# Optimization experiments

Hardware: AMD Instinct MI355X
Metric: run time of the kernel (lower is better)

Reference implementation:

```python
import jax, jax.numpy as jnp
import numpy as np

DIM = 256; QK = 256; HEADS = 8; TOPK = 2; WV = 2; WH = 2
SCALE = QK ** -0.5


def setup_inputs() -> dict:
    key = jax.random.key(0)
    ks = jax.random.split(key, 6)
    x = jax.random.normal(ks[0], (4, DIM, 64, 64), jnp.float32)
    Wqkv = jax.random.normal(ks[1], (DIM, 2 * QK + DIM), jnp.float32) * 0.02
    bqkv = jnp.zeros((2 * QK + DIM,), jnp.float32)
    Wo = jax.random.normal(ks[2], (DIM, DIM), jnp.float32) * 0.02
    bo = jnp.zeros((DIM,), jnp.float32)
    lepe_w = jax.random.normal(ks[3], (3, 3, 1, DIM), jnp.float32) * 0.1  # HWIO depthwise
    lepe_b = jnp.zeros((DIM,), jnp.float32)
    return {"x": x, "Wqkv": Wqkv, "bqkv": bqkv, "Wo": Wo, "bo": bo,
            "lepe_w": lepe_w, "lepe_b": lepe_b}


def _dwconv(x, w, b):
    # depthwise 3x3 conv, NHWC
    y = jax.lax.conv_general_dilated(x, w, (1, 1), 'SAME',
                                     dimension_numbers=('NHWC', 'HWIO', 'NHWC'),
                                     feature_group_count=x.shape[-1])
    return y + b


def _branch(win, Wqkv, bqkv, lepe_w, lepe_b, to_image):
    n, p2, h, w, _ = win.shape
    w2 = h * w
    qkv = win @ Wqkv + bqkv
    q = qkv[..., :QK]
    kv = qkv[..., QK:]                                  # [n,p2,h,w,QK+DIM]
    q_pix = q.reshape(n, p2, w2, QK)
    kv_pix = kv.reshape(n, p2, w2, QK + DIM)            # identity kv_down
    # region routing (detached in original)
    q_win = jax.lax.stop_gradient(q).mean((2, 3))       # [n,p2,QK]
    k_win = jax.lax.stop_gradient(kv[..., :QK]).mean((2, 3))
    logit = jnp.einsum('npc,nqc->npq', q_win * SCALE, k_win)
    _, r_idx = jax.lax.top_k(logit, TOPK)               # [n,p2,TOPK]
    # gather selected KV windows (mul_weight='none')
    kv_sel = jax.vmap(lambda kvb, idxb: kvb[idxb])(kv_pix, r_idx)  # [n,p2,k,w2,ckv]
    k_sel = kv_sel[..., :QK].reshape(n, p2, TOPK * w2, HEADS, QK // HEADS)
    v_sel = kv_sel[..., QK:].reshape(n, p2, TOPK * w2, HEADS, DIM // HEADS)
    qh = q_pix.reshape(n, p2, w2, HEADS, QK // HEADS)
    attn = jax.nn.softmax(jnp.einsum('npqhd,npkhd->nphqk', qh * SCALE, k_sel), axis=-1)
    out = jnp.einsum('nphqk,npkhd->npqhd', attn, v_sel).reshape(n, p2, h, w, DIM)
    lepe = _dwconv(to_image(kv[..., QK:]), lepe_w, lepe_b)
    return to_image(out) + lepe


def reference(x, Wqkv, bqkv, Wo, bo, lepe_w, lepe_b):
    xh = x.transpose(0, 2, 3, 1)                        # NHWC
    N, H, W, C = xh.shape
    v_win, h_win = H // WV, W // WH
    # vertical branch: horizontal strips of height WV, full width
    vm = xh.reshape(N, v_win, WV, W, C)
    # horizontal branch: vertical strips of width WH, full height
    hm = xh.reshape(N, H, h_win, WH, C).transpose(0, 2, 1, 3, 4)
    img_v = lambda a: a.reshape(N, H, W, a.shape[-1])
    img_h = lambda a: a.transpose(0, 2, 1, 3, 4).reshape(N, H, W, a.shape[-1])
    o1 = _branch(vm, Wqkv, bqkv, lepe_w, lepe_b, img_v)
    o2 = _branch(hm, Wqkv, bqkv, lepe_w, lepe_b, img_h)
    out = (o1 @ Wo + bo) + (o2 @ Wo + bo)
    return out.transpose(0, 3, 1, 2)                    # back to NCHW
```

## Files before the change

### kernel.cpp

```cpp
#include <hip/hip_runtime.h>
#include <hip/hip_bf16.h>
#include <math.h>

#define NBATCH 4
#define HW     4096
#define NPIX   16384
#define SCALE  0.0625f
#define QLOG2E (0.0625f * 1.44269504088896340736f)

typedef __attribute__((ext_vector_type(8))) short bf16x8;
typedef __attribute__((ext_vector_type(4))) float f32x4;

__device__ __forceinline__ int pixmap(int b, int n, int p, int pos){
  return (b == 0) ? (n*HW + p*128 + pos)
                  : (n*HW + (pos >> 1)*64 + (p << 1) + (pos & 1));
}

__device__ __forceinline__ ushort f2b(float x){
  __hip_bfloat16 h = __float2bfloat16(x);
  return *reinterpret_cast<ushort*>(&h);
}
__device__ __forceinline__ float b2f(ushort u){
  __hip_bfloat16 h = *reinterpret_cast<__hip_bfloat16*>(&u);
  return __bfloat162float(h);
}
__device__ __forceinline__ uint pk2(float a, float b){
  return (uint)f2b(a) | ((uint)f2b(b) << 16);
}

__global__ __launch_bounds__(256) void k_xt(
    const float* __restrict__ x, ushort* __restrict__ Xb)
{
  __shared__ float T[32][257];
  const int n = blockIdx.y, hw0 = blockIdx.x * 32;
  const int tid = threadIdx.x;
  const int hl = tid & 31, cg = tid >> 5;
  #pragma unroll 8
  for(int i = 0; i < 32; i++){
    const int c = i*8 + cg;
    T[hl][c] = x[((size_t)(n*256 + c))*4096 + hw0 + hl];
  }
  __syncthreads();
  const int c0 = (tid & 31)*8, pb = tid >> 5;
  #pragma unroll
  for(int i = 0; i < 4; i++){
    const int p = pb + 8*i;
    union { bf16x8 v; ushort u[8]; } U;
    #pragma unroll
    for(int j = 0; j < 8; j++) U.u[j] = f2b(T[p][c0 + j]);
    *(bf16x8*)(Xb + ((size_t)(n*HW + hw0 + p))*256 + c0) = U.v;
  }
}

__global__ __launch_bounds__(256) void k_wt(
    const float* __restrict__ Wqkv, ushort* __restrict__ Wt)
{
  const int o = blockIdx.x, t = threadIdx.x;
  Wt[(size_t)o*256 + t] = f2b(Wqkv[(size_t)t*768 + o]);
}

__global__ __launch_bounds__(256) void k_wto(
    const float* __restrict__ Wo, ushort* __restrict__ WoT)
{
  const int o = blockIdx.x, t = threadIdx.x;
  WoT[(size_t)o*256 + t] = f2b(Wo[(size_t)t*256 + o]);
}

__global__ __launch_bounds__(256) void k_qkv_mfma(
    const ushort* __restrict__ Xb, const ushort* __restrict__ Wt,
    const float* __restrict__ bqkv, ushort* __restrict__ QKVb)
{
  const int tid = threadIdx.x;
  const int l = tid & 63, w = tid >> 6;
  const int wr = w >> 1, wc = w & 1;
  const int q16 = l & 15, g = l >> 4;
  const int row0 = blockIdx.x*128 + wr*64;
  const int col0 = blockIdx.y*128 + wc*64;

  f32x4 acc[4][4];
  #pragma unroll
  for(int i = 0; i < 4; i++)
    #pragma unroll
    for(int j = 0; j < 4; j++) acc[i][j] = (f32x4){0,0,0,0};

  const ushort* Ab = Xb + (size_t)(row0 + q16)*256 + 8*g;
  const ushort* Bb = Wt + (size_t)(col0 + q16)*256 + 8*g;

  #pragma unroll
  for(int ks = 0; ks < 8; ks++){
    const int k0 = ks*32;
    bf16x8 a[4], b[4];
    #pragma unroll
    for(int i = 0; i < 4; i++) a[i] = *(const bf16x8*)(Ab + (size_t)(16*i)*256 + k0);
    #pragma unroll
    for(int j = 0; j < 4; j++) b[j] = *(const bf16x8*)(Bb + (size_t)(16*j)*256 + k0);
    #pragma unroll
    for(int i = 0; i < 4; i++)
      #pragma unroll
      for(int j = 0; j < 4; j++)
        acc[i][j] = __builtin_amdgcn_mfma_f32_16x16x32_bf16(a[i], b[j], acc[i][j], 0, 0, 0);
  }

  #pragma unroll
  for(int j = 0; j < 4; j++){
    const int col = col0 + 16*j + q16;
    const float bias = bqkv[col];
    const float sc = (col < 256) ? QLOG2E : 1.f;
    #pragma unroll
    for(int i = 0; i < 4; i++){
      #pragma unroll
      for(int r = 0; r < 4; r++){
        const int row = row0 + 16*i + 4*g + r;
        QKVb[(size_t)row*768 + col] = f2b((acc[i][j][r] + bias) * sc);
      }
    }
  }
}

__global__ __launch_bounds__(256) void k_vt(
    const ushort* __restrict__ QKVb, ushort* __restrict__ Vt)
{
  __shared__ ushort T[32][258];
  const int tile = blockIdx.x;
  const int n = tile >> 7;
  const int hw0 = (tile & 127) * 32;
  const int tid = threadIdx.x;
  #pragma unroll 4
  for(int i = 0; i < 32; i++)
    T[i][tid] = QKVb[(size_t)(n*HW + hw0 + i)*768 + 512 + tid];
  __syncthreads();
  const int px = tid & 31, wv = tid >> 5;
  #pragma unroll 4
  for(int ccb = 0; ccb < 32; ccb++){
    const int c = ccb*8 + wv;
    Vt[((size_t)(n*256 + c))*4096 + hw0 + px] = T[px][c];
  }
}

__global__ __launch_bounds__(256) void k_xmean(
    const float* __restrict__ x, float* __restrict__ xwin)
{
  const int n = blockIdx.y;
  const int c = blockIdx.x*4 + (threadIdx.x >> 6);
  const int l = threadIdx.x & 63;
  const float* xc = x + ((size_t)(n*256 + c))*4096;

  float csum = 0.f;
  for(int h = 0; h < 64; h++) csum += xc[h*64 + l];
  float rsum = 0.f;
  const float4* xr = (const float4*)(xc + l*64);
  #pragma unroll 4
  for(int i = 0; i < 16; i++){ const float4 v = xr[i]; rsum += (v.x+v.y)+(v.z+v.w); }

  const int p = l & 31;
  const float rp = __shfl(rsum, 2*p) + __shfl(rsum, 2*p + 1);
  const float cp = __shfl(csum, 2*p) + __shfl(csum, 2*p + 1);
  if(l < 32){
    xwin[((size_t)((0*NBATCH + n)*32 + p))*256 + c] = rp * (1.f/128.f);
    xwin[((size_t)((1*NBATCH + n)*32 + p))*256 + c] = cp * (1.f/128.f);
  }
}

__global__ __launch_bounds__(256) void k_win_gemm(
    const float* __restrict__ xwin, const float* __restrict__ Wqkv,
    const float* __restrict__ bqkv, float* __restrict__ qwin, float* __restrict__ kwin)
{
  __shared__ float xs[256];
  const int row = blockIdx.x;
  const int tid = threadIdx.x;
  xs[tid] = xwin[(size_t)row*256 + tid];
  __syncthreads();
  #pragma unroll
  for(int half = 0; half < 2; half++){
    const int col = half*256 + tid;
    float s = 0.f;
    for(int k = 0; k < 256; k++) s += xs[k] * Wqkv[(size_t)k*768 + col];
    s += bqkv[col];
    if(half == 0) qwin[(size_t)row*256 + tid] = s;
    else          kwin[(size_t)row*256 + tid] = s;
  }
}

__global__ __launch_bounds__(256) void k_logits_top2(
    const float* __restrict__ qwin, const float* __restrict__ kwin, int* __restrict__ ridx)
{
  const int n = blockIdx.x, b = blockIdx.y;
  __shared__ float lg[32][32];
  const int base = ((b*NBATCH + n)*32)*256;
  for(int t = threadIdx.x; t < 1024; t += 256){
    const int p = t >> 5, q = t & 31;
    const float* qp = qwin + base + p*256;
    const float* kq = kwin + base + q*256;
    float s = 0.f;
    for(int c = 0; c < 256; c++) s += qp[c]*kq[c];
    lg[p][q] = s * SCALE;
  }
  __syncthreads();
  if(threadIdx.x < 32){
    const int p = threadIdx.x;
    float m0 = -INFINITY; int i0 = 0;
    for(int q = 0; q < 32; q++){ const float v = lg[p][q]; if(v > m0){ m0 = v; i0 = q; } }
    float m1 = -INFINITY; int i1 = 0;
    for(int q = 0; q < 32; q++){ if(q == i0) continue; const float v = lg[p][q]; if(v > m1){ m1 = v; i1 = q; } }
    const int o = ((b*NBATCH + n)*32 + p)*2;
    ridx[o] = i0; ridx[o+1] = i1;
  }
}

__global__ __launch_bounds__(64) void k_attn_mfma(
    const ushort* __restrict__ QKVb, const ushort* __restrict__ Vt,
    const int* __restrict__ ridx, ushort* __restrict__ Ob)
{
  int id = blockIdx.x;
  const int hd = id & 7;  id >>= 3;
  const int p  = id & 31; id >>= 5;
  const int n  = id & 3;  id >>= 2;
  const int b  = id;
  const int l = threadIdx.x;
  const int q16 = l & 15, g = l >> 4;

  const int ro = ((b*NBATCH + n)*32 + p)*2;
  const int r0 = ridx[ro], r1 = ridx[ro+1];

  int qpix[8];
  bf16x8 qf[8];
  #pragma unroll
  for(int m = 0; m < 8; m++){
    qpix[m] = pixmap(b, n, p, m*16 + q16);
    qf[m] = *(const bf16x8*)(QKVb + (size_t)qpix[m]*768 + hd*32 + 8*g);
  }

  f32x4 acc0[8], acc1[8];
  float rs[8];
  #pragma unroll
  for(int m = 0; m < 8; m++){
    acc0[m] = (f32x4){0,0,0,0}; acc1[m] = (f32x4){0,0,0,0}; rs[m] = 0.f;
  }

  const int e = g & 1, t = g >> 1;
  const int a0 = (q16 + 32*e) << 2;
  const int a1 = (q16 + 32*e + 16) << 2;

  for(int c = 0; c < 8; c++){
    const int wsel = (c < 4) ? r0 : r1;
    const int posb = (32*c) & 127;

    bf16x8 kf0, kf1;
    {
      const int kp0 = pixmap(b, n, wsel, posb + q16);
      kf0 = *(const bf16x8*)(QKVb + (size_t)kp0*768 + 256 + hd*32 + 8*g);
      const int kp1 = pixmap(b, n, wsel, posb + 16 + q16);
      kf1 = *(const bf16x8*)(QKVb + (size_t)kp1*768 + 256 + hd*32 + 8*g);
    }
    bf16x8 vf0, vf1;
    if(b == 0){
      const ushort* base = Vt + ((size_t)(n*256 + hd*32 + q16))*4096 + wsel*128 + posb + 8*g;
      vf0 = *(const bf16x8*)base;
      vf1 = *(const bf16x8*)(base + (size_t)16*4096);
    } else {
      const int h0 = (posb + 8*g) >> 1;
      const ushort* base = Vt + ((size_t)(n*256 + hd*32 + q16))*4096 + h0*64 + 2*wsel;
      union { bf16x8 v; uint u[4]; } U0, U1;
      #pragma unroll
      for(int j = 0; j < 4; j++){
        U0.u[j] = *(const uint*)(base + j*64);
        U1.u[j] = *(const uint*)(base + (size_t)16*4096 + j*64);
      }
      vf0 = U0.v; vf1 = U1.v;
    }

    #pragma unroll
    for(int m = 0; m < 8; m++){
      const f32x4 z = {0,0,0,0};
      f32x4 s0 = __builtin_amdgcn_mfma_f32_16x16x32_bf16(kf0, qf[m], z, 0, 0, 0);
      f32x4 s1 = __builtin_amdgcn_mfma_f32_16x16x32_bf16(kf1, qf[m], z, 0, 0, 0);
      float p00 = exp2f(s0[0]), p01 = exp2f(s0[1]), p02 = exp2f(s0[2]), p03 = exp2f(s0[3]);
      float p10 = exp2f(s1[0]), p11 = exp2f(s1[1]), p12 = exp2f(s1[2]), p13 = exp2f(s1[3]);
      rs[m] += ((p00+p01)+(p02+p03)) + ((p10+p11)+(p12+p13));
      const uint w00 = pk2(p00, p01), w01 = pk2(p02, p03);
      const uint w10 = pk2(p10, p11), w11 = pk2(p12, p13);
      const uint x00 = (uint)__builtin_amdgcn_ds_bpermute(a0, (int)w00);
      const uint x01 = (uint)__builtin_amdgcn_ds_bpermute(a0, (int)w01);
      const uint x10 = (uint)__builtin_amdgcn_ds_bpermute(a0, (int)w10);
      const uint x11 = (uint)__builtin_amdgcn_ds_bpermute(a0, (int)w11);
      const uint y00 = (uint)__builtin_amdgcn_ds_bpermute(a1, (int)w00);
      const uint y01 = (uint)__builtin_amdgcn_ds_bpermute(a1, (int)w01);
      const uint y10 = (uint)__builtin_amdgcn_ds_bpermute(a1, (int)w10);
      const uint y11 = (uint)__builtin_amdgcn_ds_bpermute(a1, (int)w11);
      union { bf16x8 v; uint u[4]; } P;
      P.u[0] = t ? x10 : x00;
      P.u[1] = t ? x11 : x01;
      P.u[2] = t ? y10 : y00;
      P.u[3] = t ? y11 : y01;
      acc0[m] = __builtin_amdgcn_mfma_f32_16x16x32_bf16(vf0, P.v, acc0[m], 0, 0, 0);
      acc1[m] = __builtin_amdgcn_mfma_f32_16x16x32_bf16(vf1, P.v, acc1[m], 0, 0, 0);
    }
  }

  #pragma unroll
  for(int m = 0; m < 8; m++){
    float r = rs[m];
    r += __shfl_xor(r, 16);
    r += __shfl_xor(r, 32);
    rs[m] = 1.f / r;
  }
  #pragma unroll
  for(int m = 0; m < 8; m++){
    ushort* op = Ob + ((size_t)b*NPIX + qpix[m])*256 + hd*32 + 4*g;
    const float iv = rs[m];
    ushort4 o0 = { f2b(acc0[m][0]*iv), f2b(acc0[m][1]*iv), f2b(acc0[m][2]*iv), f2b(acc0[m][3]*iv) };
    ushort4 o1 = { f2b(acc1[m][0]*iv), f2b(acc1[m][1]*iv), f2b(acc1[m][2]*iv), f2b(acc1[m][3]*iv) };
    *(ushort4*)op = o0;
    *(ushort4*)(op + 16) = o1;
  }
}

__global__ __launch_bounds__(256) void k_combine_lepe(
    const ushort* __restrict__ QKVb, const ushort* __restrict__ Ob0,
    const ushort* __restrict__ Ob1,
    const float* __restrict__ lw, const float* __restrict__ lb, ushort* __restrict__ Sb)
{
  const int pix = blockIdx.x;
  const int c = threadIdx.x;
  const int n = pix >> 12, rem = pix & 4095;
  const int h = rem >> 6, w = rem & 63;
  float conv = 0.f;
  #pragma unroll
  for(int kh = 0; kh < 3; kh++){
    const int hh = h + kh - 1;
    if(hh < 0 || hh >= 64) continue;
    #pragma unroll
    for(int kw = 0; kw < 3; kw++){
      const int wi = w + kw - 1;
      if(wi < 0 || wi >= 64) continue;
      const int np = (n*64 + hh)*64 + wi;
      conv += b2f(QKVb[(size_t)np*768 + 512 + c]) * lw[(kh*3 + kw)*256 + c];
    }
  }
  const size_t idx = (size_t)pix*256 + c;
  Sb[idx] = f2b(b2f(Ob0[idx]) + b2f(Ob1[idx]) + 2.f*(conv + lb[c]));
}

__global__ __launch_bounds__(256) void k_out_mfma(
    const ushort* __restrict__ Sb, const ushort* __restrict__ WoT,
    const float* __restrict__ bo, float* __restrict__ out)
{
  const int tid = threadIdx.x;
  const int l = tid & 63, w = tid >> 6;
  const int wr = w >> 1, wc = w & 1;
  const int q16 = l & 15, g = l >> 4;
  const int c0   = blockIdx.x*128 + wr*64;
  const int pix0 = blockIdx.y*128 + wc*64;
  const int n = pix0 >> 12, rem0 = pix0 & 4095;

  f32x4 acc[4][4];
  #pragma unroll
  for(int i = 0; i < 4; i++)
    #pragma unroll
    for(int j = 0; j < 4; j++) acc[i][j] = (f32x4){0,0,0,0};

  const ushort* Ab = WoT + (size_t)(c0 + q16)*256 + 8*g;
  const ushort* Bb = Sb  + (size_t)(pix0 + q16)*256 + 8*g;

  #pragma unroll
  for(int ks = 0; ks < 8; ks++){
    const int k0 = ks*32;
    bf16x8 a[4], b[4];
    #pragma unroll
    for(int i = 0; i < 4; i++) a[i] = *(const bf16x8*)(Ab + (size_t)(16*i)*256 + k0);
    #pragma unroll
    for(int j = 0; j < 4; j++) b[j] = *(const bf16x8*)(Bb + (size_t)(16*j)*256 + k0);
    #pragma unroll
    for(int i = 0; i < 4; i++)
      #pragma unroll
      for(int j = 0; j < 4; j++)
        acc[i][j] = __builtin_amdgcn_mfma_f32_16x16x32_bf16(a[i], b[j], acc[i][j], 0, 0, 0);
  }

  float* outn = out + (size_t)n*256*4096;
  #pragma unroll
  for(int i = 0; i < 4; i++){
    #pragma unroll
    for(int r = 0; r < 4; r++){
      const int c = c0 + 16*i + 4*g + r;
      const float bias = 2.f*bo[c];
      #pragma unroll
      for(int j = 0; j < 4; j++){
        const int rem = rem0 + 16*j + q16;
        outn[(size_t)c*4096 + rem] = acc[i][j][r] + bias;
      }
    }
  }
}

extern "C" void kernel_launch(void* const* d_in, const int* in_sizes, int n_in,
                              void* d_out, int out_size, void* d_ws, size_t ws_size,
                              hipStream_t stream)
{
  const float* x    = (const float*)d_in[0];
  const float* Wqkv = (const float*)d_in[1];
  const float* bqkv = (const float*)d_in[2];
  const float* Wo   = (const float*)d_in[3];
  const float* bo   = (const float*)d_in[4];
  const float* lw   = (const float*)d_in[5];
  const float* lb   = (const float*)d_in[6];
  float* out = (float*)d_out;

  char* w = (char*)d_ws;
  ushort* Xb   = (ushort*)w; w += (size_t)NPIX*256*2;
  ushort* Wt   = (ushort*)w; w += (size_t)768*256*2;
  ushort* WoT  = (ushort*)w; w += (size_t)256*256*2;
  ushort* QKVb = (ushort*)w; w += (size_t)NPIX*768*2;
  ushort* Vt   = (ushort*)w; w += (size_t)NPIX*256*2;
  ushort* Ob   = (ushort*)w; w += (size_t)2*NPIX*256*2;
  ushort* Sb   = (ushort*)w; w += (size_t)NPIX*256*2;
  float*  xwin = (float*)w;  w += (size_t)2*NBATCH*32*256*4;
  float*  qwin = (float*)w;  w += (size_t)2*NBATCH*32*256*4;
  float*  kwin = (float*)w;  w += (size_t)2*NBATCH*32*256*4;
  int*    ridx = (int*)w;    w += (size_t)2*NBATCH*32*2*4;

  ushort* Ob0 = Ob;
  ushort* Ob1 = Ob + (size_t)NPIX*256;

  k_xt          <<<dim3(128,NBATCH), 256, 0, stream>>>(x, Xb);
  k_wt          <<<768, 256, 0, stream>>>(Wqkv, Wt);
  k_wto         <<<256, 256, 0, stream>>>(Wo, WoT);
  k_qkv_mfma    <<<dim3(128,6), 256, 0, stream>>>(Xb, Wt, bqkv, QKVb);
  k_vt          <<<512, 256, 0, stream>>>(QKVb, Vt);
  k_xmean       <<<dim3(64,NBATCH), 256, 0, stream>>>(x, xwin);
  k_win_gemm    <<<256, 256, 0, stream>>>(xwin, Wqkv, bqkv, qwin, kwin);
  k_logits_top2 <<<dim3(NBATCH,2), 256, 0, stream>>>(qwin, kwin, ridx);
  k_attn_mfma   <<<2048, 64, 0, stream>>>(QKVb, Vt, ridx, Ob);
  k_combine_lepe<<<NPIX, 256, 0, stream>>>(QKVb, Ob0, Ob1, lw, lb, Sb);
  k_out_mfma    <<<dim3(2,128), 256, 0, stream>>>(Sb, WoT, bo, out);
}
```

Before: 191.1 us.

## Remove P-matrix lane permutes by reordering V loads; pack 4 waves per block

The attention kernel no longer shuffles the exponentiated scores across lanes with ds_bpermute before the PV MFMA. Instead it loads the V fragments in a permuted key order, split into two half-vectors at offsets matched to the score layout, so the packed scores can feed the MFMA directly. It also launches four independent 64-lane wavefronts per 256-thread block instead of one per block. Separately, the window-mean kernel computes column sums from the row-wise float4 loads plus wave-level xor-shuffle reductions, replacing a strided column loop. The trade is smaller, more scattered V loads and many shuffles in the mean kernel.

```diff
diff --git a/kernel.cpp b/kernel.cpp
--- a/kernel.cpp
+++ b/kernel.cpp
@@ -145,16 +145,38 @@
   const int l = threadIdx.x & 63;
   const float* xc = x + ((size_t)(n*256 + c))*4096;
 
-  float csum = 0.f;
-  for(int h = 0; h < 64; h++) csum += xc[h*64 + l];
+  float4 cs[8];
+  #pragma unroll
+  for(int i = 0; i < 8; i++) cs[i] = (float4){0,0,0,0};
   float rsum = 0.f;
   const float4* xr = (const float4*)(xc + l*64);
-  #pragma unroll 4
-  for(int i = 0; i < 16; i++){ const float4 v = xr[i]; rsum += (v.x+v.y)+(v.z+v.w); }
-
+  #pragma unroll
+  for(int i = 0; i < 16; i++){
+    const float4 v = xr[i];
+    rsum += (v.x+v.y)+(v.z+v.w);
+    const float p0 = v.x+v.y, p1 = v.z+v.w;
+    if(i & 1){ cs[i>>1].z += p0; cs[i>>1].w += p1; }
+    else     { cs[i>>1].x += p0; cs[i>>1].y += p1; }
+  }
+  #pragma unroll
+  for(int i = 0; i < 8; i++){
+    #pragma unroll
+    for(int s = 1; s < 64; s <<= 1){
+      cs[i].x += __shfl_xor(cs[i].x, s);
+      cs[i].y += __shfl_xor(cs[i].y, s);
+      cs[i].z += __shfl_xor(cs[i].z, s);
+      cs[i].w += __shfl_xor(cs[i].w, s);
+    }
+  }
   const int p = l & 31;
   const float rp = __shfl(rsum, 2*p) + __shfl(rsum, 2*p + 1);
-  const float cp = __shfl(csum, 2*p) + __shfl(csum, 2*p + 1);
+  float cp;
+  {
+    const int hi = p >> 2, lo = p & 3;
+    const float4 q = hi==0?cs[0]:hi==1?cs[1]:hi==2?cs[2]:hi==3?cs[3]
+                   : hi==4?cs[4]:hi==5?cs[5]:hi==6?cs[6]:cs[7];
+    cp = lo==0?q.x : lo==1?q.y : lo==2?q.z : q.w;
+  }
   if(l < 32){
     xwin[((size_t)((0*NBATCH + n)*32 + p))*256 + c] = rp * (1.f/128.f);
     xwin[((size_t)((1*NBATCH + n)*32 + p))*256 + c] = cp * (1.f/128.f);
@@ -207,16 +229,16 @@
   }
 }
 
-__global__ __launch_bounds__(64) void k_attn_mfma(
+__global__ __launch_bounds__(256) void k_attn_mfma(
     const ushort* __restrict__ QKVb, const ushort* __restrict__ Vt,
     const int* __restrict__ ridx, ushort* __restrict__ Ob)
 {
-  int id = blockIdx.x;
+  int id = blockIdx.x*4 + (threadIdx.x >> 6);
   const int hd = id & 7;  id >>= 3;
   const int p  = id & 31; id >>= 5;
   const int n  = id & 3;  id >>= 2;
   const int b  = id;
-  const int l = threadIdx.x;
+  const int l = threadIdx.x & 63;
   const int q16 = l & 15, g = l >> 4;
 
   const int ro = ((b*NBATCH + n)*32 + p)*2;
@@ -236,10 +258,6 @@
   for(int m = 0; m < 8; m++){
     acc0[m] = (f32x4){0,0,0,0}; acc1[m] = (f32x4){0,0,0,0}; rs[m] = 0.f;
   }
-
-  const int e = g & 1, t = g >> 1;
-  const int a0 = (q16 + 32*e) << 2;
-  const int a1 = (q16 + 32*e + 16) << 2;
 
   for(int c = 0; c < 8; c++){
     const int wsel = (c < 4) ? r0 : r1;
@@ -254,18 +272,26 @@
     }
     bf16x8 vf0, vf1;
     if(b == 0){
-      const ushort* base = Vt + ((size_t)(n*256 + hd*32 + q16))*4096 + wsel*128 + posb + 8*g;
-      vf0 = *(const bf16x8*)base;
-      vf1 = *(const bf16x8*)(base + (size_t)16*4096);
+      const ushort* base = Vt + ((size_t)(n*256 + hd*32 + q16))*4096 + wsel*128 + posb + 4*g;
+      union { bf16x8 v; ushort4 h[2]; } U0, U1;
+      U0.h[0] = *(const ushort4*)(base);
+      U0.h[1] = *(const ushort4*)(base + 16);
+      U1.h[0] = *(const ushort4*)(base + (size_t)16*4096);
+      U1.h[1] = *(const ushort4*)(base + (size_t)16*4096 + 16);
+      vf0 = U0.v; vf1 = U1.v;
     } else {
-      const int h0 = (posb + 8*g) >> 1;
-      const ushort* base = Vt + ((size_t)(n*256 + hd*32 + q16))*4096 + h0*64 + 2*wsel;
+      const int h0 = (posb + 4*g) >> 1;
+      const ushort* base = Vt + ((size_t)(n*256 + hd*32 + q16))*4096 + 2*wsel;
       union { bf16x8 v; uint u[4]; } U0, U1;
-      #pragma unroll
-      for(int j = 0; j < 4; j++){
-        U0.u[j] = *(const uint*)(base + j*64);
-        U1.u[j] = *(const uint*)(base + (size_t)16*4096 + j*64);
-      }
+      U0.u[0] = *(const uint*)(base + (h0    )*64);
+      U0.u[1] = *(const uint*)(base + (h0 + 1)*64);
+      U0.u[2] = *(const uint*)(base + (h0 + 8)*64);
+      U0.u[3] = *(const uint*)(base + (h0 + 9)*64);
+      const ushort* base1 = base + (size_t)16*4096;
+      U1.u[0] = *(const uint*)(base1 + (h0    )*64);
+      U1.u[1] = *(const uint*)(base1 + (h0 + 1)*64);
+      U1.u[2] = *(const uint*)(base1 + (h0 + 8)*64);
+      U1.u[3] = *(const uint*)(base1 + (h0 + 9)*64);
       vf0 = U0.v; vf1 = U1.v;
     }
 
@@ -274,24 +300,14 @@
       const f32x4 z = {0,0,0,0};
       f32x4 s0 = __builtin_amdgcn_mfma_f32_16x16x32_bf16(kf0, qf[m], z, 0, 0, 0);
       f32x4 s1 = __builtin_amdgcn_mfma_f32_16x16x32_bf16(kf1, qf[m], z, 0, 0, 0);
-      float p00 = exp2f(s0[0]), p01 = exp2f(s0[1]), p02 = exp2f(s0[2]), p03 = exp2f(s0[3]);
-      float p10 = exp2f(s1[0]), p11 = exp2f(s1[1]), p12 = exp2f(s1[2]), p13 = exp2f(s1[3]);
-      rs[m] += ((p00+p01)+(p02+p03)) + ((p10+p11)+(p12+p13));
-      const uint w00 = pk2(p00, p01), w01 = pk2(p02, p03);
-      const uint w10 = pk2(p10, p11), w11 = pk2(p12, p13);
-      const uint x00 = (uint)__builtin_amdgcn_ds_bpermute(a0, (int)w00);
-      const uint x01 = (uint)__builtin_amdgcn_ds_bpermute(a0, (int)w01);
-      const uint x10 = (uint)__builtin_amdgcn_ds_bpermute(a0, (int)w10);
-      const uint x11 = (uint)__builtin_amdgcn_ds_bpermute(a0, (int)w11);
-      const uint y00 = (uint)__builtin_amdgcn_ds_bpermute(a1, (int)w00);
-      const uint y01 = (uint)__builtin_amdgcn_ds_bpermute(a1, (int)w01);
-      const uint y10 = (uint)__builtin_amdgcn_ds_bpermute(a1, (int)w10);
-      const uint y11 = (uint)__builtin_amdgcn_ds_bpermute(a1, (int)w11);
+      const float e00 = exp2f(s0[0]), e01 = exp2f(s0[1]), e02 = exp2f(s0[2]), e03 = exp2f(s0[3]);
+      const float e10 = exp2f(s1[0]), e11 = exp2f(s1[1]), e12 = exp2f(s1[2]), e13 = exp2f(s1[3]);
+      rs[m] += ((e00+e01)+(e02+e03)) + ((e10+e11)+(e12+e13));
       union { bf16x8 v; uint u[4]; } P;
-      P.u[0] = t ? x10 : x00;
-      P.u[1] = t ? x11 : x01;
-      P.u[2] = t ? y10 : y00;
-      P.u[3] = t ? y11 : y01;
+      P.u[0] = pk2(e00, e01);
+      P.u[1] = pk2(e02, e03);
+      P.u[2] = pk2(e10, e11);
+      P.u[3] = pk2(e12, e13);
       acc0[m] = __builtin_amdgcn_mfma_f32_16x16x32_bf16(vf0, P.v, acc0[m], 0, 0, 0);
       acc1[m] = __builtin_amdgcn_mfma_f32_16x16x32_bf16(vf1, P.v, acc1[m], 0, 0, 0);
     }
@@ -430,7 +446,7 @@
   k_xmean       <<<dim3(64,NBATCH), 256, 0, stream>>>(x, xwin);
   k_win_gemm    <<<256, 256, 0, stream>>>(xwin, Wqkv, bqkv, qwin, kwin);
   k_logits_top2 <<<dim3(NBATCH,2), 256, 0, stream>>>(qwin, kwin, ridx);
-  k_attn_mfma   <<<2048, 64, 0, stream>>>(QKVb, Vt, ridx, Ob);
+  k_attn_mfma   <<<512, 256, 0, stream>>>(QKVb, Vt, ridx, Ob);
   k_combine_lepe<<<NPIX, 256, 0, stream>>>(QKVb, Ob0, Ob1, lw, lb, Sb);
   k_out_mfma    <<<dim3(2,128), 256, 0, stream>>>(Sb, WoT, bo, out);
 }
```

Measured after the change: 190.3 us. Within noise of the previous version (-0.4%).
